# Performance work log

Hardware: AMD Instinct MI355X
Metric: run time of the kernel (lower is better)

## Reference

```python
import jax, jax.numpy as jnp
import numpy as np
import math

B, T, M, C, H = 2, 2048, 77, 512, 8
D = C // H  # head dim = 64


def setup_inputs() -> dict:
    key = jax.random.key(0)
    ks = jax.random.split(key, 20)
    s = 0.02
    inp = {
        "x": jax.random.normal(ks[0], (B, T, C), jnp.float32),
        "c": jax.random.normal(ks[1], (B, M, C), jnp.float32),
        # causal mask for self-attention (masked_fill where == 0)
        "attn_mask": jnp.tril(jnp.ones((T, T), jnp.int32))[None, None],
        "padding_mask": jnp.ones((B, M), jnp.int32),
    }
    names = ["Wq", "Wk", "Wv", "Wkc", "Wvc", "Wg1", "Wg2", "Wp"]
    for i, n in enumerate(names):
        inp[n] = jax.random.normal(ks[2 + i], (C, C), jnp.float32) * s
        inp["b" + n[1:]] = jnp.zeros((C,), jnp.float32)
    return inp


def _heads(t):
    # [B, S, C] -> [B, S, H, D]
    return t.reshape(t.shape[0], t.shape[1], H, D)


def reference(x, c, attn_mask, padding_mask,
              Wq, bq, Wk, bk, Wv, bv, Wkc, bkc, Wvc, bvc,
              Wg1, bg1, Wg2, bg2, Wp, bp):
    scale = 1.0 / math.sqrt(D)
    q = _heads(x @ Wq + bq)      # [B,T,H,D]
    k = _heads(x @ Wk + bk)      # [B,T,H,D]
    v = _heads(x @ Wv + bv)
    k_c = _heads(c @ Wkc + bkc)  # [B,M,H,D]
    v_c = _heads(c @ Wvc + bvc)

    # self-attention branch
    att = jnp.einsum("bthd,bshd->bhts", q, k) * scale   # [B,H,T,T]
    att = jnp.where(attn_mask == 0, -jnp.inf, att)
    att = jax.nn.softmax(att, axis=-1)
    y = jnp.einsum("bhts,bshd->bthd", att, v).reshape(B, T, C)

    # cross-attention branch to condition c
    att_c = jnp.einsum("bthd,bmhd->bhtm", q, k_c) * scale  # [B,H,T,M]
    att_c = jnp.where(padding_mask[:, None, None, :] == 0, -jnp.inf, att_c)
    att_c = jax.nn.softmax(att_c, axis=-1)
    y_c = jnp.einsum("bhtm,bmhd->bthd", att_c, v_c).reshape(B, T, C)

    # sigmoid gating fusion (note: gates cross-multiply branches, per source)
    gate_self = jax.nn.sigmoid(y @ Wg1 + bg1)
    gate_c = jax.nn.sigmoid(y_c @ Wg2 + bg2)
    y = gate_self * y_c + gate_c * y
    return y @ Wp + bp
```

## Files before the change

kernel.cpp:

```cpp
#include <hip/hip_runtime.h>
#include <hip/hip_bf16.h>
#include <math.h>

#define BB 2
#define TT 2048
#define MM 77
#define CC 512
#define HH 8
#define DD 64

typedef short bf16x8 __attribute__((ext_vector_type(8)));
typedef float f32x4  __attribute__((ext_vector_type(4)));

static __device__ __forceinline__ unsigned short f2bf(float x) {
    __hip_bfloat16 h = __float2bfloat16(x);
    return *reinterpret_cast<unsigned short*>(&h);
}
static __device__ __forceinline__ float bf2f(unsigned short u) {
    unsigned int v = ((unsigned int)u) << 16;
    return *reinterpret_cast<float*>(&v);
}

__global__ __launch_bounds__(256)
void wconv8(const float* __restrict__ w0, const float* __restrict__ w1,
            const float* __restrict__ w2, const float* __restrict__ w3,
            const float* __restrict__ w4, const float* __restrict__ w5,
            const float* __restrict__ w6, const float* __restrict__ w7,
            unsigned short* __restrict__ outbase)
{
    const float* W;
    switch (blockIdx.z) {
        case 0: W = w0; break; case 1: W = w1; break;
        case 2: W = w2; break; case 3: W = w3; break;
        case 4: W = w4; break; case 5: W = w5; break;
        case 6: W = w6; break; default: W = w7; break;
    }
    unsigned short* Wp = outbase + (size_t)blockIdx.z * 512 * 512;
    const int k0 = blockIdx.x * 64;
    const int n0 = blockIdx.y * 64;
    const int tid = threadIdx.x;
    __shared__ unsigned short t[64 * 72];

    #pragma unroll
    for (int it = 0; it < 4; ++it) {
        const int e = tid + 256 * it;
        const int r  = e >> 4;
        const int c4 = (e & 15) * 4;
        const float4 v = *(const float4*)(W + (size_t)(k0 + r) * 512 + n0 + c4);
        t[(c4 + 0) * 72 + r] = f2bf(v.x);
        t[(c4 + 1) * 72 + r] = f2bf(v.y);
        t[(c4 + 2) * 72 + r] = f2bf(v.z);
        t[(c4 + 3) * 72 + r] = f2bf(v.w);
    }
    __syncthreads();
    #pragma unroll
    for (int it = 0; it < 2; ++it) {
        const int e    = tid + 256 * it;
        const int gl   = e >> 7;
        const int ktl  = (e >> 6) & 1;
        const int lane = e & 63;
        const int l15  = lane & 15;
        const int q    = lane >> 4;
        const int4 v = *(const int4*)&t[(gl * 16 + l15) * 72 + ktl * 32 + q * 8];
        const int G  = (n0 >> 4) + gl;
        const int KT = (k0 >> 5) + ktl;
        *(int4*)(Wp + ((size_t)(G * 16 + KT) * 64 + lane) * 8) = v;
    }
}

__global__ __launch_bounds__(256)
void proj_all(const float* __restrict__ x, const float* __restrict__ cin,
              const unsigned short* __restrict__ Wt8,
              const float* __restrict__ bq, const float* __restrict__ bk,
              const float* __restrict__ bv, const float* __restrict__ bkc,
              const float* __restrict__ bvc,
              unsigned short* __restrict__ qb, unsigned short* __restrict__ kcb)
{
    __shared__ unsigned short As[2 * 16 * 64 * 8];

    const int tid = threadIdx.x;
    int b = blockIdx.x;
    const float* Ap; const unsigned short* Wtp;
    const float *bb0, *bb1, *bb2;
    unsigned short* outb;
    int row0, colb, N, S, whichStride;
    float oscale;
    if (b < 768) {
        row0 = (b & 127) * 32; colb = (b >> 7) * 256;
        Ap = x; Wtp = Wt8; N = BB * TT; S = TT;
        whichStride = 2097152; oscale = 0.125f;
        outb = qb; bb0 = bq; bb1 = bk; bb2 = bv;
    } else {
        b -= 768;
        row0 = (b % 5) * 32; colb = (b / 5) * 256;
        Ap = cin; Wtp = Wt8 + 3 * 262144; N = BB * MM; S = MM;
        whichStride = 131072; oscale = 1.0f;
        outb = kcb; bb0 = bkc; bb1 = bvc; bb2 = nullptr;
    }

    {
        const int r    = tid >> 3;
        const int rg   = r >> 4;
        const int l15r = r & 15;
        const int seg  = (tid & 7) * 64;
        const int gr   = row0 + r;
        unsigned short tmp[64];
        #pragma unroll
        for (int j = 0; j < 16; ++j) {
            float4 v = (gr < N) ? *(const float4*)(Ap + (size_t)gr * 512 + seg + j * 4)
                                : make_float4(0.f, 0.f, 0.f, 0.f);
            tmp[j*4+0] = f2bf(v.x); tmp[j*4+1] = f2bf(v.y);
            tmp[j*4+2] = f2bf(v.z); tmp[j*4+3] = f2bf(v.w);
        }
        #pragma unroll
        for (int jb = 0; jb < 8; ++jb) {
            const int k  = seg + jb * 8;
            const int kt = k >> 5;
            const int q  = (k >> 3) & 3;
            *(int4*)&As[((rg * 16 + kt) * 64 + q * 16 + l15r) * 8] = *(int4*)&tmp[jb*8];
        }
    }
    __syncthreads();

    const int wv   = tid >> 6;
    const int lane = tid & 63;
    const int l15  = lane & 15;
    const int quad = lane >> 4;
    const int wc   = colb + wv * 64;
    const int wcg  = wc >> 4;

    f32x4 acc[2][4];
    #pragma unroll
    for (int mi = 0; mi < 2; ++mi)
        #pragma unroll
        for (int ni = 0; ni < 4; ++ni) acc[mi][ni] = (f32x4){0.f, 0.f, 0.f, 0.f};

    bf16x8 b0v[4], b1v[4], b2v[4];
    #pragma unroll
    for (int ni = 0; ni < 4; ++ni) {
        b0v[ni] = *(const bf16x8*)(Wtp + (((size_t)(wcg + ni) * 16 + 0) << 9) + lane * 8);
        b1v[ni] = *(const bf16x8*)(Wtp + (((size_t)(wcg + ni) * 16 + 1) << 9) + lane * 8);
    }

    for (int kt = 0; kt < 16; ++kt) {
        if (kt + 2 < 16) {
            #pragma unroll
            for (int ni = 0; ni < 4; ++ni)
                b2v[ni] = *(const bf16x8*)(Wtp + (((size_t)(wcg + ni) * 16 + kt + 2) << 9) + lane * 8);
        }
        const bf16x8 a0 = *(const bf16x8*)&As[((0 * 16 + kt) * 64 + lane) * 8];
        const bf16x8 a1 = *(const bf16x8*)&As[((1 * 16 + kt) * 64 + lane) * 8];
        #pragma unroll
        for (int ni = 0; ni < 4; ++ni) {
            acc[0][ni] = __builtin_amdgcn_mfma_f32_16x16x32_bf16(a0, b0v[ni], acc[0][ni], 0, 0, 0);
            acc[1][ni] = __builtin_amdgcn_mfma_f32_16x16x32_bf16(a1, b0v[ni], acc[1][ni], 0, 0, 0);
        }
        #pragma unroll
        for (int ni = 0; ni < 4; ++ni) { b0v[ni] = b1v[ni]; b1v[ni] = b2v[ni]; }
    }

    const int which = wc >> 9;
    const float* bsel = (which == 0) ? bb0 : ((which == 1) ? bb1 : bb2);
    const float sc = (which == 0) ? oscale : 1.f;
    unsigned short* dst = outb + (size_t)which * whichStride;

    float bvv[4];
    #pragma unroll
    for (int ni = 0; ni < 4; ++ni)
        bvv[ni] = bsel[(wc + ni * 16 + l15) & 511];

    #pragma unroll
    for (int mi = 0; mi < 2; ++mi) {
        #pragma unroll
        for (int reg = 0; reg < 4; ++reg) {
            const int row = row0 + mi * 16 + quad * 4 + reg;
            if (row >= N) continue;
            const int b_ = row / S;
            const int s_ = row - b_ * S;
            #pragma unroll
            for (int ni = 0; ni < 4; ++ni) {
                const float v = (acc[mi][ni][reg] + bvv[ni]) * sc;
                const int cl = (wc + ni * 16 + l15) & 511;
                dst[((size_t)(b_ * HH + (cl >> 6)) * S + s_) * DD + (cl & 63)] = f2bf(v);
            }
        }
    }
}

template<int ACT, int OUT, int AMODE>
__global__ __launch_bounds__(256)
void gemm_rs(const void* __restrict__ A0, const void* __restrict__ A1,
             const void* __restrict__ A2, const void* __restrict__ A3,
             const unsigned short* __restrict__ Wt,
             const float* __restrict__ b0, const float* __restrict__ b1,
             void* __restrict__ out0, void* __restrict__ out1,
             int N, int NC)
{
    __shared__ unsigned short As[2 * 16 * 64 * 8];

    const int tid  = threadIdx.x;
    const int z    = blockIdx.z;
    const int row0 = blockIdx.x * 32;
    const int colb = blockIdx.y * 256;
    const void* Ap = z ? A1 : A0;

    {
        const int r    = tid >> 3;
        const int rg   = r >> 4;
        const int l15r = r & 15;
        const int seg  = (tid & 7) * 64;
        const int gr   = row0 + r;
        unsigned short tmp[64];
        if (AMODE == 2) {
            #pragma unroll
            for (int jb = 0; jb < 8; ++jb) {
                unsigned short a[8], bq_[8], c[8], d[8];
                if (gr < N) {
                    const size_t off = (size_t)gr * 512 + seg + jb * 8;
                    *(int4*)a   = *(const int4*)((const unsigned short*)A0 + off);
                    *(int4*)bq_ = *(const int4*)((const unsigned short*)A1 + off);
                    *(int4*)c   = *(const int4*)((const unsigned short*)A2 + off);
                    *(int4*)d   = *(const int4*)((const unsigned short*)A3 + off);
                    #pragma unroll
                    for (int k = 0; k < 8; ++k)
                        tmp[jb*8+k] = f2bf(bf2f(a[k]) * bf2f(bq_[k]) + bf2f(c[k]) * bf2f(d[k]));
                } else {
                    #pragma unroll
                    for (int k = 0; k < 8; ++k) tmp[jb*8+k] = 0;
                }
            }
        } else {
            const unsigned short* Ab = (const unsigned short*)Ap;
            #pragma unroll
            for (int jb = 0; jb < 8; ++jb) {
                int4 v = (gr < N) ? *(const int4*)(Ab + (size_t)gr * 512 + seg + jb * 8)
                                  : make_int4(0, 0, 0, 0);
                *(int4*)&tmp[jb*8] = v;
            }
        }
        #pragma unroll
        for (int jb = 0; jb < 8; ++jb) {
            const int k  = seg + jb * 8;
            const int kt = k >> 5;
            const int q  = (k >> 3) & 3;
            *(int4*)&As[((rg * 16 + kt) * 64 + q * 16 + l15r) * 8] = *(int4*)&tmp[jb*8];
        }
    }
    __syncthreads();

    const int wv   = tid >> 6;
    const int lane = tid & 63;
    const int l15  = lane & 15;
    const int quad = lane >> 4;
    const int wc   = colb + wv * 64;
    const int wcg  = wc >> 4;

    f32x4 acc[2][4];
    #pragma unroll
    for (int mi = 0; mi < 2; ++mi)
        #pragma unroll
        for (int ni = 0; ni < 4; ++ni) acc[mi][ni] = (f32x4){0.f, 0.f, 0.f, 0.f};

    const unsigned short* Wz = Wt + (size_t)z * NC;

    bf16x8 b0v[4], b1v[4], b2v[4];
    #pragma unroll
    for (int ni = 0; ni < 4; ++ni) {
        b0v[ni] = *(const bf16x8*)(Wz + (((size_t)(wcg + ni) * 16 + 0) << 9) + lane * 8);
        b1v[ni] = *(const bf16x8*)(Wz + (((size_t)(wcg + ni) * 16 + 1) << 9) + lane * 8);
    }

    for (int kt = 0; kt < 16; ++kt) {
        if (kt + 2 < 16) {
            #pragma unroll
            for (int ni = 0; ni < 4; ++ni)
                b2v[ni] = *(const bf16x8*)(Wz + (((size_t)(wcg + ni) * 16 + kt + 2) << 9) + lane * 8);
        }
        const bf16x8 a0 = *(const bf16x8*)&As[((0 * 16 + kt) * 64 + lane) * 8];
        const bf16x8 a1 = *(const bf16x8*)&As[((1 * 16 + kt) * 64 + lane) * 8];
        #pragma unroll
        for (int ni = 0; ni < 4; ++ni) {
            acc[0][ni] = __builtin_amdgcn_mfma_f32_16x16x32_bf16(a0, b0v[ni], acc[0][ni], 0, 0, 0);
            acc[1][ni] = __builtin_amdgcn_mfma_f32_16x16x32_bf16(a1, b0v[ni], acc[1][ni], 0, 0, 0);
        }
        #pragma unroll
        for (int ni = 0; ni < 4; ++ni) { b0v[ni] = b1v[ni]; b1v[ni] = b2v[ni]; }
    }

    const float* bsel = ((OUT == 1) && z) ? b1 : b0;
    float bvv[4];
    #pragma unroll
    for (int ni = 0; ni < 4; ++ni)
        bvv[ni] = bsel[(wc + ni * 16 + l15) & 511];

    #pragma unroll
    for (int mi = 0; mi < 2; ++mi) {
        #pragma unroll
        for (int reg = 0; reg < 4; ++reg) {
            const int row = row0 + mi * 16 + quad * 4 + reg;
            if (row >= N) continue;
            #pragma unroll
            for (int ni = 0; ni < 4; ++ni) {
                float v = acc[mi][ni][reg] + bvv[ni];
                if (ACT == 1) v = 1.f / (1.f + __expf(-v));
                const int col = wc + ni * 16 + l15;
                if (OUT == 0) {
                    ((float*)out0)[(size_t)row * 512 + col] = v;
                } else {
                    unsigned short* dst = (unsigned short*)(z ? out1 : out0);
                    dst[(size_t)row * 512 + col] = f2bf(v);
                }
            }
        }
    }
}

__global__ __launch_bounds__(256)
void transpose_all(const unsigned short* __restrict__ vin, unsigned short* __restrict__ vout,
                   const unsigned short* __restrict__ cin_, unsigned short* __restrict__ cout_)
{
    const int bx = blockIdx.x;
    const int bh = blockIdx.y;
    const unsigned short* in; unsigned short* outp;
    int S, W, s0;
    if (bx < 32) { in = vin;  outp = vout;  S = TT; W = TT;  s0 = bx * 64; }
    else         { in = cin_; outp = cout_; S = MM; W = 128; s0 = (bx - 32) * 64; }

    const int tid = threadIdx.x;
    __shared__ unsigned short t[64 * 80];

    #pragma unroll
    for (int it = 0; it < 2; ++it) {
        const int e = tid + 256 * it;
        const int row = e >> 3;
        const int blk = e & 7;
        int4 v = make_int4(0, 0, 0, 0);
        const int s = s0 + row;
        if (s < S) v = *(const int4*)(in + ((size_t)bh * S + s) * 64 + blk * 8);
        *(int4*)&t[row * 80 + ((blk ^ (row & 7)) * 8)] = v;
    }
    __syncthreads();
    #pragma unroll
    for (int it = 0; it < 2; ++it) {
        const int e = tid + 256 * it;
        const int d  = e >> 3;
        const int kb = e & 7;
        const int key0 = s0 + kb * 8;
        if (key0 < W) {
            unsigned short tmp[8];
            #pragma unroll
            for (int j = 0; j < 8; ++j) {
                const int kl = kb * 8 + j;
                tmp[j] = t[kl * 80 + (((d >> 3) ^ (kl & 7)) * 8) + (d & 7)];
            }
            *(int4*)(outp + ((size_t)bh * 64 + d) * W + key0) = *(int4*)tmp;
        }
    }
}

__global__ __launch_bounds__(256)
void attn_all(const unsigned short* __restrict__ Qh,
              const unsigned short* __restrict__ Kh,
              const unsigned short* __restrict__ Vth,
              unsigned short* __restrict__ yout,
              const unsigned short* __restrict__ Kch,
              const unsigned short* __restrict__ Vtch,
              unsigned short* __restrict__ ycout)
{
    int lin = blockIdx.x;
    int causal, S_kv, W, bh, qt;
    const unsigned short *Kb, *Vb;
    unsigned short* outp;
    if (lin < 512) {
        causal = 1; S_kv = TT; W = TT;
        bh = (lin & 7) | (((lin >> 3) & 1) << 3);
        const int qtr = lin >> 4;
        qt = (qtr < 16) ? (31 - qtr) : (qtr - 16);
        Kb = Kh + (size_t)bh * S_kv * 64;
        Vb = Vth + (size_t)bh * 64 * W;
        outp = yout;
    } else {
        lin -= 512;
        causal = 0; S_kv = MM; W = 128;
        bh = (lin & 7) | (((lin >> 3) & 1) << 3);
        qt = lin >> 4;
        Kb = Kch + (size_t)bh * S_kv * 64;
        Vb = Vtch + (size_t)bh * 64 * W;
        outp = ycout;
    }
    const int n_kt = causal ? (qt + 1) : 2;

    const int tid  = threadIdx.x;
    const int wv   = tid >> 6;
    const int lane = tid & 63;
    const int l15  = lane & 15;
    const int quad = lane >> 4;

    __shared__ unsigned short Ks[2][64 * 80];
    __shared__ unsigned short Vs[2][64 * 80];
    __shared__ unsigned short PT[4 * 16 * 72];

    const int t0 = qt * 64 + wv * 16;
    const unsigned short* qptr = Qh + ((size_t)bh * TT + t0 + l15) * 64 + quad * 8;
    const bf16x8 qb0 = *(const bf16x8*)(qptr);
    const bf16x8 qb1 = *(const bf16x8*)(qptr + 32);

    f32x4 Oacc[4];
    #pragma unroll
    for (int dt = 0; dt < 4; ++dt) Oacc[dt] = (f32x4){0.f, 0.f, 0.f, 0.f};
    float l = 0.f;

    int4 kR[2], vR[2];
    {
        #pragma unroll
        for (int it = 0; it < 2; ++it) {
            const int e = tid + 256 * it;
            const int row = e >> 3, blk = e & 7;
            kR[it] = (row < S_kv)
                ? *(const int4*)(Kb + (size_t)row * 64 + blk * 8) : make_int4(0,0,0,0);
            vR[it] = (blk * 8 < W)
                ? *(const int4*)(Vb + (size_t)row * W + blk * 8) : make_int4(0,0,0,0);
        }
        #pragma unroll
        for (int it = 0; it < 2; ++it) {
            const int e = tid + 256 * it;
            const int row = e >> 3, blk = e & 7;
            *(int4*)&Ks[0][row * 80 + ((blk ^ (row & 7)) * 8)] = kR[it];
            *(int4*)&Vs[0][row * 80 + ((blk ^ (row & 7)) * 8)] = vR[it];
        }
    }
    __syncthreads();

    for (int kt = 0; kt < n_kt; ++kt) {
        const int buf = kt & 1;
        const int s0 = kt * 64;

        if (kt + 1 < n_kt) {
            const int s1 = (kt + 1) * 64;
            #pragma unroll
            for (int it = 0; it < 2; ++it) {
                const int e = tid + 256 * it;
                const int row = e >> 3, blk = e & 7;
                const int s = s1 + row;
                kR[it] = (s < S_kv)
                    ? *(const int4*)(Kb + (size_t)s * 64 + blk * 8) : make_int4(0,0,0,0);
                vR[it] = (s1 + blk * 8 < W)
                    ? *(const int4*)(Vb + (size_t)row * W + s1 + blk * 8) : make_int4(0,0,0,0);
            }
        }

        f32x4 sacc[4];
        __builtin_amdgcn_s_setprio(1);
        #pragma unroll
        for (int mt = 0; mt < 4; ++mt) {
            const int krow = 16 * mt + l15;
            const bf16x8 ka0 = *(const bf16x8*)&Ks[buf][krow * 80 + (((quad    ) ^ (krow & 7)) * 8)];
            const bf16x8 ka1 = *(const bf16x8*)&Ks[buf][krow * 80 + (((quad + 4) ^ (krow & 7)) * 8)];
            sacc[mt] = (f32x4){0.f, 0.f, 0.f, 0.f};
            sacc[mt] = __builtin_amdgcn_mfma_f32_16x16x32_bf16(ka0, qb0, sacc[mt], 0, 0, 0);
            sacc[mt] = __builtin_amdgcn_mfma_f32_16x16x32_bf16(ka1, qb1, sacc[mt], 0, 0, 0);
        }
        __builtin_amdgcn_s_setprio(0);

        float sv[16];
        #pragma unroll
        for (int mt = 0; mt < 4; ++mt)
            #pragma unroll
            for (int reg = 0; reg < 4; ++reg)
                sv[mt * 4 + reg] = sacc[mt][reg];

        const bool cmask = (causal && kt == qt);
        if (cmask || (s0 + 64 > S_kv)) {
            const int lim = cmask ? (t0 + l15) : 0x7fffffff;
            #pragma unroll
            for (int mt = 0; mt < 4; ++mt)
                #pragma unroll
                for (int reg = 0; reg < 4; ++reg) {
                    const int kg = s0 + 16 * mt + quad * 4 + reg;
                    if (kg > lim || kg >= S_kv) sv[mt * 4 + reg] = -INFINITY;
                }
        }

        float p[16], psum = 0.f;
        #pragma unroll
        for (int i = 0; i < 16; ++i) { p[i] = __expf(sv[i]); psum += p[i]; }
        psum += __shfl_xor(psum, 16);
        psum += __shfl_xor(psum, 32);
        l += psum;

        unsigned short* ptw = &PT[wv * 16 * 72 + l15 * 72];
        #pragma unroll
        for (int mt = 0; mt < 4; ++mt) {
            ushort4 u;
            u.x = f2bf(p[mt * 4 + 0]); u.y = f2bf(p[mt * 4 + 1]);
            u.z = f2bf(p[mt * 4 + 2]); u.w = f2bf(p[mt * 4 + 3]);
            *(ushort4*)(ptw + 16 * mt + quad * 4) = u;
        }
        const bf16x8 pb0 = *(const bf16x8*)(ptw + quad * 8);
        const bf16x8 pb1 = *(const bf16x8*)(ptw + quad * 8 + 32);

        __builtin_amdgcn_s_setprio(1);
        #pragma unroll
        for (int dt = 0; dt < 4; ++dt) {
            const int vrow = 16 * dt + l15;
            const bf16x8 va0 = *(const bf16x8*)&Vs[buf][vrow * 80 + (((quad    ) ^ (vrow & 7)) * 8)];
            const bf16x8 va1 = *(const bf16x8*)&Vs[buf][vrow * 80 + (((quad + 4) ^ (vrow & 7)) * 8)];
            Oacc[dt] = __builtin_amdgcn_mfma_f32_16x16x32_bf16(va0, pb0, Oacc[dt], 0, 0, 0);
            Oacc[dt] = __builtin_amdgcn_mfma_f32_16x16x32_bf16(va1, pb1, Oacc[dt], 0, 0, 0);
        }
        __builtin_amdgcn_s_setprio(0);

        if (kt + 1 < n_kt) {
            const int nbuf = buf ^ 1;
            #pragma unroll
            for (int it = 0; it < 2; ++it) {
                const int e = tid + 256 * it;
                const int row = e >> 3, blk = e & 7;
                *(int4*)&Ks[nbuf][row * 80 + ((blk ^ (row & 7)) * 8)] = kR[it];
                *(int4*)&Vs[nbuf][row * 80 + ((blk ^ (row & 7)) * 8)] = vR[it];
            }
        }
        __syncthreads();
    }

    const int b = bh >> 3, h = bh & 7;
    const float inv_l = 1.f / l;
    const int t = t0 + l15;
    unsigned short* ob = outp + ((size_t)b * TT + t) * CC + h * DD + quad * 4;
    #pragma unroll
    for (int dt = 0; dt < 4; ++dt) {
        ushort4 u;
        u.x = f2bf(Oacc[dt][0] * inv_l);
        u.y = f2bf(Oacc[dt][1] * inv_l);
        u.z = f2bf(Oacc[dt][2] * inv_l);
        u.w = f2bf(Oacc[dt][3] * inv_l);
        *(ushort4*)(ob + 16 * dt) = u;
    }
}

extern "C" void kernel_launch(void* const* d_in, const int* in_sizes, int n_in,
                              void* d_out, int out_size, void* d_ws, size_t ws_size,
                              hipStream_t stream)
{
    const float* x   = (const float*)d_in[0];
    const float* cin = (const float*)d_in[1];
    const float* Wq  = (const float*)d_in[4];   const float* bq  = (const float*)d_in[5];
    const float* Wk  = (const float*)d_in[6];   const float* bk  = (const float*)d_in[7];
    const float* Wv  = (const float*)d_in[8];   const float* bv  = (const float*)d_in[9];
    const float* Wkc = (const float*)d_in[10];  const float* bkc = (const float*)d_in[11];
    const float* Wvc = (const float*)d_in[12];  const float* bvc = (const float*)d_in[13];
    const float* Wg1 = (const float*)d_in[14];  const float* bg1 = (const float*)d_in[15];
    const float* Wg2 = (const float*)d_in[16];  const float* bg2 = (const float*)d_in[17];
    const float* Wp  = (const float*)d_in[18];  const float* bp  = (const float*)d_in[19];

    float* out = (float*)d_out;
    char*  w   = (char*)d_ws;
    const size_t MB = 1024 * 1024;

    unsigned short* Wt8  = (unsigned short*)(w);
    unsigned short* qb   = (unsigned short*)(w + 4  * MB);
    unsigned short* kb   = (unsigned short*)(w + 8  * MB);
    unsigned short* vb   = (unsigned short*)(w + 12 * MB);
    unsigned short* vtb  = (unsigned short*)(w + 16 * MB);
    unsigned short* yb   = (unsigned short*)(w + 20 * MB);
    unsigned short* ycb  = (unsigned short*)(w + 24 * MB);
    unsigned short* g1b  = (unsigned short*)(w + 28 * MB);
    unsigned short* g2b  = (unsigned short*)(w + 32 * MB);
    unsigned short* kcb  = (unsigned short*)(w + 40 * MB);
    unsigned short* vcb  = (unsigned short*)(w + 40 * MB + 256 * 1024);
    unsigned short* vtcb = (unsigned short*)(w + 40 * MB + 512 * 1024);

    const dim3 blk(256);

    wconv8<<<dim3(8, 8, 8), blk, 0, stream>>>(Wq, Wk, Wv, Wkc, Wvc, Wg1, Wg2, Wp, Wt8);

    proj_all<<<dim3(788), blk, 0, stream>>>(
        x, cin, Wt8, bq, bk, bv, bkc, bvc, qb, kcb);

    transpose_all<<<dim3(34, BB * HH), blk, 0, stream>>>(vb, vtb, vcb, vtcb);

    attn_all<<<dim3(1024), blk, 0, stream>>>(qb, kb, vtb, yb, kcb, vtcb, ycb);

    gemm_rs<1, 1, 0><<<dim3(128, 2, 2), blk, 0, stream>>>(
        yb, ycb, nullptr, nullptr, Wt8 + 5 * 262144, bg1, bg2, g1b, g2b,
        BB * TT, 262144);

    gemm_rs<0, 0, 2><<<dim3(128, 2), blk, 0, stream>>>(
        g1b, ycb, g2b, yb, Wt8 + 7 * 262144, bp, nullptr, out, nullptr,
        BB * TT, 0);
}
```

Before: 204.6 us.

## Fuse V transpose into projection epilogue and drop transpose kernel

The projection kernel now stages its output tile through shared memory and writes Q/K rows with vectorised stores. V is written directly in transposed [B,H,D,T] layout, and the cross-attention Vc is written transposed with its zero padding. This removes the separate transpose kernel launch and the round trip of V through global memory. It adds a block-level sync and LDS staging in the epilogue, reusing the A-tile shared buffer.

Result: no change. 202.5 us (-1.0%).

```diff
diff --git a/kernel.cpp b/kernel.cpp
--- a/kernel.cpp
+++ b/kernel.cpp
@@ -74,7 +74,10 @@
               const float* __restrict__ bq, const float* __restrict__ bk,
               const float* __restrict__ bv, const float* __restrict__ bkc,
               const float* __restrict__ bvc,
-              unsigned short* __restrict__ qb, unsigned short* __restrict__ kcb)
+              unsigned short* __restrict__ qb,
+              unsigned short* __restrict__ vtb,
+              unsigned short* __restrict__ kcb,
+              unsigned short* __restrict__ vtcb)
 {
     __shared__ unsigned short As[2 * 16 * 64 * 8];
 
@@ -82,20 +85,20 @@
     int b = blockIdx.x;
     const float* Ap; const unsigned short* Wtp;
     const float *bb0, *bb1, *bb2;
-    unsigned short* outb;
-    int row0, colb, N, S, whichStride;
+    int row0, colb, N, isSelf;
     float oscale;
     if (b < 768) {
+        isSelf = 1;
         row0 = (b & 127) * 32; colb = (b >> 7) * 256;
-        Ap = x; Wtp = Wt8; N = BB * TT; S = TT;
-        whichStride = 2097152; oscale = 0.125f;
-        outb = qb; bb0 = bq; bb1 = bk; bb2 = bv;
+        Ap = x; Wtp = Wt8; N = BB * TT;
+        oscale = 0.125f;
+        bb0 = bq; bb1 = bk; bb2 = bv;
     } else {
-        b -= 768;
+        b -= 768; isSelf = 0;
         row0 = (b % 5) * 32; colb = (b / 5) * 256;
-        Ap = cin; Wtp = Wt8 + 3 * 262144; N = BB * MM; S = MM;
-        whichStride = 131072; oscale = 1.0f;
-        outb = kcb; bb0 = bkc; bb1 = bvc; bb2 = nullptr;
+        Ap = cin; Wtp = Wt8 + 3 * 262144; N = BB * MM;
+        oscale = 1.0f;
+        bb0 = bkc; bb1 = bvc; bb2 = nullptr;
     }
 
     {
@@ -162,26 +165,90 @@
     const int which = wc >> 9;
     const float* bsel = (which == 0) ? bb0 : ((which == 1) ? bb1 : bb2);
     const float sc = (which == 0) ? oscale : 1.f;
-    unsigned short* dst = outb + (size_t)which * whichStride;
 
     float bvv[4];
     #pragma unroll
     for (int ni = 0; ni < 4; ++ni)
         bvv[ni] = bsel[(wc + ni * 16 + l15) & 511];
 
-    #pragma unroll
-    for (int mi = 0; mi < 2; ++mi) {
-        #pragma unroll
-        for (int reg = 0; reg < 4; ++reg) {
-            const int row = row0 + mi * 16 + quad * 4 + reg;
-            if (row >= N) continue;
-            const int b_ = row / S;
-            const int s_ = row - b_ * S;
-            #pragma unroll
-            for (int ni = 0; ni < 4; ++ni) {
-                const float v = (acc[mi][ni][reg] + bvv[ni]) * sc;
-                const int cl = (wc + ni * 16 + l15) & 511;
-                dst[((size_t)(b_ * HH + (cl >> 6)) * S + s_) * DD + (cl & 63)] = f2bf(v);
+    if (isSelf) {
+        const int b_ = row0 >> 11;
+        const int t0 = row0 & 2047;
+        const int h  = (wc & 511) >> 6;
+        __syncthreads();
+        if (which < 2) {
+            unsigned short* TL = (unsigned short*)As + wv * (32 * 72);
+            #pragma unroll
+            for (int mi = 0; mi < 2; ++mi)
+                #pragma unroll
+                for (int ni = 0; ni < 4; ++ni)
+                    #pragma unroll
+                    for (int reg = 0; reg < 4; ++reg) {
+                        const int t = mi * 16 + quad * 4 + reg;
+                        const int d = ni * 16 + l15;
+                        TL[t * 72 + d] = f2bf((acc[mi][ni][reg] + bvv[ni]) * sc);
+                    }
+            unsigned short* dst = qb + (size_t)which * 2097152
+                                + (((size_t)b_ * 8 + h) * 2048 + t0) * 64;
+            #pragma unroll
+            for (int it = 0; it < 4; ++it) {
+                const int t = it * 8 + (lane >> 3);
+                *(int4*)(dst + (size_t)t * 64 + (lane & 7) * 8)
+                    = *(const int4*)&TL[t * 72 + (lane & 7) * 8];
+            }
+        } else {
+            unsigned short* TL = (unsigned short*)As + wv * (64 * 40);
+            #pragma unroll
+            for (int mi = 0; mi < 2; ++mi)
+                #pragma unroll
+                for (int ni = 0; ni < 4; ++ni) {
+                    ushort4 u;
+                    u.x = f2bf(acc[mi][ni][0] + bvv[ni]);
+                    u.y = f2bf(acc[mi][ni][1] + bvv[ni]);
+                    u.z = f2bf(acc[mi][ni][2] + bvv[ni]);
+                    u.w = f2bf(acc[mi][ni][3] + bvv[ni]);
+                    const int d = ni * 16 + l15;
+                    *(ushort4*)&TL[d * 40 + mi * 16 + quad * 4] = u;
+                }
+            unsigned short* dst = vtb + (((size_t)b_ * 8 + h) * 64) * 2048 + t0;
+            #pragma unroll
+            for (int it = 0; it < 4; ++it) {
+                const int d = it * 16 + (lane >> 2);
+                *(int4*)(dst + (size_t)d * 2048 + (lane & 3) * 8)
+                    = *(const int4*)&TL[d * 40 + (lane & 3) * 8];
+            }
+        }
+    } else {
+        #pragma unroll
+        for (int mi = 0; mi < 2; ++mi)
+            #pragma unroll
+            for (int reg = 0; reg < 4; ++reg) {
+                const int row = row0 + mi * 16 + quad * 4 + reg;
+                if (row >= N) continue;
+                const int b_ = (row >= MM) ? 1 : 0;
+                const int m_ = row - b_ * MM;
+                #pragma unroll
+                for (int ni = 0; ni < 4; ++ni) {
+                    const float v = acc[mi][ni][reg] + bvv[ni];
+                    const int cl = (wc + ni * 16 + l15) & 511;
+                    const int hh = cl >> 6, d = cl & 63;
+                    if (which == 0)
+                        kcb[(((size_t)b_ * 8 + hh) * 77 + m_) * 64 + d] = f2bf(v);
+                    else
+                        vtcb[(((size_t)b_ * 8 + hh) * 64 + d) * 128 + m_] = f2bf(v);
+                }
+            }
+        if (which == 1 && row0 == 0) {
+            const int h0 = (colb - 512) >> 6;
+            for (int e = tid; e < 2 * 4 * 64; e += 256) {
+                const int d  = e & 63;
+                const int hl = (e >> 6) & 3;
+                const int bz = e >> 8;
+                unsigned short* rp = vtcb + (((size_t)bz * 8 + h0 + hl) * 64 + d) * 128;
+                rp[77] = 0; rp[78] = 0; rp[79] = 0;
+                #pragma unroll
+                for (int q8 = 80; q8 < 128; q8 += 8)
+                    *(int4*)(rp + q8) = make_int4(0, 0, 0, 0);
             }
         }
     }
@@ -311,49 +378,6 @@
                     dst[(size_t)row * 512 + col] = f2bf(v);
                 }
             }
-        }
-    }
-}
-
-__global__ __launch_bounds__(256)
-void transpose_all(const unsigned short* __restrict__ vin, unsigned short* __restrict__ vout,
-                   const unsigned short* __restrict__ cin_, unsigned short* __restrict__ cout_)
-{
-    const int bx = blockIdx.x;
-    const int bh = blockIdx.y;
-    const unsigned short* in; unsigned short* outp;
-    int S, W, s0;
-    if (bx < 32) { in = vin;  outp = vout;  S = TT; W = TT;  s0 = bx * 64; }
-    else         { in = cin_; outp = cout_; S = MM; W = 128; s0 = (bx - 32) * 64; }
-
-    const int tid = threadIdx.x;
-    __shared__ unsigned short t[64 * 80];
-
-    #pragma unroll
-    for (int it = 0; it < 2; ++it) {
-        const int e = tid + 256 * it;
-        const int row = e >> 3;
-        const int blk = e & 7;
-        int4 v = make_int4(0, 0, 0, 0);
-        const int s = s0 + row;
-        if (s < S) v = *(const int4*)(in + ((size_t)bh * S + s) * 64 + blk * 8);
-        *(int4*)&t[row * 80 + ((blk ^ (row & 7)) * 8)] = v;
-    }
-    __syncthreads();
-    #pragma unroll
-    for (int it = 0; it < 2; ++it) {
-        const int e = tid + 256 * it;
-        const int d  = e >> 3;
-        const int kb = e & 7;
-        const int key0 = s0 + kb * 8;
-        if (key0 < W) {
-            unsigned short tmp[8];
-            #pragma unroll
-            for (int j = 0; j < 8; ++j) {
-                const int kl = kb * 8 + j;
-                tmp[j] = t[kl * 80 + (((d >> 3) ^ (kl & 7)) * 8) + (d & 7)];
-            }
-            *(int4*)(outp + ((size_t)bh * 64 + d) * W + key0) = *(int4*)tmp;
         }
     }
 }
@@ -559,15 +583,12 @@
 
     unsigned short* Wt8  = (unsigned short*)(w);
     unsigned short* qb   = (unsigned short*)(w + 4  * MB);
-    unsigned short* kb   = (unsigned short*)(w + 8  * MB);
-    unsigned short* vb   = (unsigned short*)(w + 12 * MB);
     unsigned short* vtb  = (unsigned short*)(w + 16 * MB);
     unsigned short* yb   = (unsigned short*)(w + 20 * MB);
     unsigned short* ycb  = (unsigned short*)(w + 24 * MB);
     unsigned short* g1b  = (unsigned short*)(w + 28 * MB);
     unsigned short* g2b  = (unsigned short*)(w + 32 * MB);
     unsigned short* kcb  = (unsigned short*)(w + 40 * MB);
-    unsigned short* vcb  = (unsigned short*)(w + 40 * MB + 256 * 1024);
     unsigned short* vtcb = (unsigned short*)(w + 40 * MB + 512 * 1024);
 
     const dim3 blk(256);
@@ -575,11 +596,10 @@
     wconv8<<<dim3(8, 8, 8), blk, 0, stream>>>(Wq, Wk, Wv, Wkc, Wvc, Wg1, Wg2, Wp, Wt8);
 
     proj_all<<<dim3(788), blk, 0, stream>>>(
-        x, cin, Wt8, bq, bk, bv, bkc, bvc, qb, kcb);
-
-    transpose_all<<<dim3(34, BB * HH), blk, 0, stream>>>(vb, vtb, vcb, vtcb);
-
-    attn_all<<<dim3(1024), blk, 0, stream>>>(qb, kb, vtb, yb, kcb, vtcb, ycb);
+        x, cin, Wt8, bq, bk, bv, bkc, bvc, qb, vtb, kcb, vtcb);
+
+    attn_all<<<dim3(1024), blk, 0, stream>>>(
+        qb, qb + 2097152, vtb, yb, kcb, vtcb, ycb);
 
     gemm_rs<1, 1, 0><<<dim3(128, 2, 2), blk, 0, stream>>>(
         yb, ycb, nullptr, nullptr, Wt8 + 5 * 262144, bg1, bg2, g1b, g2b,
```
